# Optimization experiments

Hardware: AMD Instinct MI355X
Metric: run time of the kernel (lower is better)

## Reference

```python
import jax, jax.numpy as jnp
import numpy as np

N = 100_000          # nodes
E = 3_200_000        # train edges (avg degree 32)
E_TEST = 500_000     # pos/neg test edges each
F_IN, F_HID, F_OUT = 256, 16, 64


def setup_inputs() -> dict:
    key = jax.random.key(0)
    ks = jax.random.split(key, 7)
    x = jax.random.normal(ks[0], (N, F_IN), jnp.float32)
    train_edge_index = jax.random.randint(ks[1], (2, E), 0, N, dtype=jnp.int32)
    test_pos_edge_index = jax.random.randint(ks[2], (2, E_TEST), 0, N, dtype=jnp.int32)
    test_neg_edge_index = jax.random.randint(ks[3], (2, E_TEST), 0, N, dtype=jnp.int32)
    W1 = jax.random.normal(ks[4], (F_IN, F_HID), jnp.float32) / np.float32(np.sqrt(F_IN))
    b1 = jnp.zeros((F_HID,), jnp.float32)
    W2 = jax.random.normal(ks[5], (F_HID, F_OUT), jnp.float32) / np.float32(np.sqrt(F_HID))
    b2 = jnp.zeros((F_OUT,), jnp.float32)
    return dict(x=x, train_edge_index=train_edge_index,
                test_pos_edge_index=test_pos_edge_index,
                test_neg_edge_index=test_neg_edge_index,
                W1=W1, b1=b1, W2=W2, b2=b2)


def gcn_conv(x, edge_index, W, b, n):
    """PyG GCNConv: x' = D^-1/2 (A+I) D^-1/2 (x W) + b (self-loops added)."""
    h = x @ W                                  # project first (PyG order)
    loop = jnp.arange(n, dtype=edge_index.dtype)
    src = jnp.concatenate([edge_index[0], loop])
    dst = jnp.concatenate([edge_index[1], loop])
    deg = jax.ops.segment_sum(jnp.ones_like(dst, dtype=h.dtype), dst, num_segments=n)
    dinv = jnp.where(deg > 0, jax.lax.rsqrt(deg), 0.0)
    norm = dinv[src] * dinv[dst]               # per-edge symmetric norm
    msg = h[src] * norm[:, None]               # gather + scale
    out = jax.ops.segment_sum(msg, dst, num_segments=n)  # scatter-add
    return out + b


def reference(x, train_edge_index, test_pos_edge_index, test_neg_edge_index,
              W1, b1, W2, b2):
    n = x.shape[0]
    z = gcn_conv(x, train_edge_index, W1, b1, n)
    z = jax.nn.relu(z)
    z = gcn_conv(z, train_edge_index, W2, b2, n)
    edge_index = jnp.concatenate([test_pos_edge_index, test_neg_edge_index], axis=-1)
    logits = jnp.sum(z[edge_index[0]] * z[edge_index[1]], axis=-1)
    return logits
```

## Files before the change

kernel.cpp:

```cpp
#include <hip/hip_runtime.h>


#define CAP   18432
#define CHUNK 4096

__global__ void seed_kernel(int* __restrict__ gtail, int nb1) {
    int t = blockIdx.x * blockDim.x + threadIdx.x;
    if (t < nb1) gtail[t] = t * CAP;
}

__global__ void prep_kernel(const float* __restrict__ W2, const float* __restrict__ b2,
                            float* __restrict__ mw) {
    int t = threadIdx.x;
    int r = t >> 4, cc = t & 15;
    float s = 0.0f;
    for (int j = 0; j < 64; ++j) s += W2[r * 64 + j] * W2[cc * 64 + j];
    mw[t] = s;
    if (t < 16) {
        float w = 0.0f;
        for (int j = 0; j < 64; ++j) w += W2[t * 64 + j] * b2[j];
        mw[256 + t] = w;
    }
    if (t == 0) {
        float bbv = 0.0f;
        for (int j = 0; j < 64; ++j) bbv += b2[j] * b2[j];
        mw[272] = bbv;
    }
}

__global__ void passA1_kernel(const int* __restrict__ src, const int* __restrict__ dst, int E,
                              int* __restrict__ gtail, unsigned* __restrict__ tmp, int nb1) {
    __shared__ int cnt[256];
    __shared__ int base[256];
    int t = threadIdx.x;
    int c0 = blockIdx.x * CHUNK;
    if (t < nb1) cnt[t] = 0;
    __syncthreads();
    unsigned rec[16];
    unsigned brk[16];
    #pragma unroll
    for (int j = 0; j < 16; ++j) {
        int e = c0 + t + j * 256;
        if (e < E) {
            int s = src[e], d = dst[e];
            int b = d >> 9;
            int r = atomicAdd(&cnt[b], 1);
            rec[j] = (unsigned)s | ((unsigned)(d & 511) << 20);
            brk[j] = ((unsigned)b << 16) | (unsigned)r;
        }
    }
    __syncthreads();
    if (t < nb1) base[t] = atomicAdd(&gtail[t], cnt[t]);
    __syncthreads();
    #pragma unroll
    for (int j = 0; j < 16; ++j) {
        int e = c0 + t + j * 256;
        if (e < E) {
            int b = (int)(brk[j] >> 16), r = (int)(brk[j] & 0xFFFFu);
            tmp[base[b] + r] = rec[j];
        }
    }
}

__global__ void fill2_kernel(const int* __restrict__ gtail, const unsigned* __restrict__ tmp,
                             int* __restrict__ eidx, int* __restrict__ rowptr,
                             int* __restrict__ counts, float* __restrict__ dinv, int n) {
    int b = blockIdx.x;
    int t = threadIdx.x;
    int beg = b * CAP;
    int cnt_total = gtail[b] - beg;
    __shared__ int h[512];
    __shared__ int cur[512];
    h[t] = 0; h[t + 256] = 0;
    __syncthreads();
    for (int i = t; i < cnt_total; i += 256) {
        unsigned r = tmp[beg + i];
        atomicAdd(&h[r >> 20], 1);
    }
    __syncthreads();
    if (t == 0) {
        int run = beg;
        for (int j = 0; j < 512; ++j) { int c = h[j]; cur[j] = run; run += c; }
    }
    __syncthreads();
    for (int j = t; j < 512; j += 256) {
        int v = (b << 9) + j;
        if (v < n) {
            rowptr[v] = cur[j];
            counts[v] = h[j];
            dinv[v]   = rsqrtf((float)h[j] + 1.0f);
        }
    }
    __syncthreads();
    for (int i = t; i < cnt_total; i += 256) {
        unsigned r = tmp[beg + i];
        int p = atomicAdd(&cur[r >> 20], 1);
        eidx[p] = (int)(r & 0xFFFFF);
    }
}

__global__ void gemm1_kernel(const float* __restrict__ x, const float* __restrict__ W1,
                             const float* __restrict__ dinv, float* __restrict__ hs, int n) {
    __shared__ float4 sW[1024];
    const float4* W14 = (const float4*)W1;
    for (int i = threadIdx.x; i < 1024; i += 256) sW[i] = W14[i];
    __syncthreads();
    int row = blockIdx.x * 256 + threadIdx.x;
    if (row >= n) return;
    const float4* x4 = (const float4*)(x + (size_t)row * 256);
    float4 a0 = {0,0,0,0}, a1 = {0,0,0,0}, a2 = {0,0,0,0}, a3 = {0,0,0,0};
    for (int k4 = 0; k4 < 64; ++k4) {
        float4 xv = x4[k4];
        #pragma unroll
        for (int j = 0; j < 4; ++j) {
            float xk = (j == 0) ? xv.x : (j == 1) ? xv.y : (j == 2) ? xv.z : xv.w;
            int k = (k4 << 2) + j;
            float4 w0 = sW[k * 4 + 0];
            float4 w1 = sW[k * 4 + 1];
            float4 w2 = sW[k * 4 + 2];
            float4 w3 = sW[k * 4 + 3];
            a0.x += xk * w0.x; a0.y += xk * w0.y; a0.z += xk * w0.z; a0.w += xk * w0.w;
            a1.x += xk * w1.x; a1.y += xk * w1.y; a1.z += xk * w1.z; a1.w += xk * w1.w;
            a2.x += xk * w2.x; a2.y += xk * w2.y; a2.z += xk * w2.z; a2.w += xk * w2.w;
            a3.x += xk * w3.x; a3.y += xk * w3.y; a3.z += xk * w3.z; a3.w += xk * w3.w;
        }
    }
    float di = dinv[row];
    float4* o = (float4*)(hs + (size_t)row * 16);
    a0.x *= di; a0.y *= di; a0.z *= di; a0.w *= di;
    a1.x *= di; a1.y *= di; a1.z *= di; a1.w *= di;
    a2.x *= di; a2.y *= di; a2.z *= di; a2.w *= di;
    a3.x *= di; a3.y *= di; a3.z *= di; a3.w *= di;
    o[0] = a0; o[1] = a1; o[2] = a2; o[3] = a3;
}

__global__ void agg1_kernel(const int* __restrict__ rowptr, const int* __restrict__ counts,
                            const int* __restrict__ eidx, const float4* __restrict__ hs4,
                            const float* __restrict__ dinv, const float* __restrict__ b1,
                            float4* __restrict__ gs4, int n) {
    int t = blockIdx.x * blockDim.x + threadIdx.x;
    int v = t >> 3;
    if (v >= n) return;
    int q = t & 3, hh = (t >> 2) & 1;
    int start = rowptr[v], cnt = counts[v];
    float4 s = {0, 0, 0, 0};
    int i = hh;
    for (; i + 6 < cnt; i += 8) {
        int s0 = eidx[start + i];
        int s1 = eidx[start + i + 2];
        int s2 = eidx[start + i + 4];
        int s3 = eidx[start + i + 6];
        float4 h0 = hs4[(size_t)s0 * 4 + q];
        float4 h1 = hs4[(size_t)s1 * 4 + q];
        float4 h2 = hs4[(size_t)s2 * 4 + q];
        float4 h3 = hs4[(size_t)s3 * 4 + q];
        s.x += h0.x + h1.x + h2.x + h3.x;
        s.y += h0.y + h1.y + h2.y + h3.y;
        s.z += h0.z + h1.z + h2.z + h3.z;
        s.w += h0.w + h1.w + h2.w + h3.w;
    }
    for (; i < cnt; i += 2) {
        float4 h0 = hs4[(size_t)eidx[start + i] * 4 + q];
        s.x += h0.x; s.y += h0.y; s.z += h0.z; s.w += h0.w;
    }
    s.x += __shfl_xor(s.x, 4);
    s.y += __shfl_xor(s.y, 4);
    s.z += __shfl_xor(s.z, 4);
    s.w += __shfl_xor(s.w, 4);
    if (hh == 0) {
        float di = dinv[v];
        float4 h = hs4[(size_t)v * 4 + q];
        float4 b = ((const float4*)b1)[q];
        float4 z;
        z.x = fmaxf(di * (s.x + h.x) + b.x, 0.0f) * di;
        z.y = fmaxf(di * (s.y + h.y) + b.y, 0.0f) * di;
        z.z = fmaxf(di * (s.z + h.z) + b.z, 0.0f) * di;
        z.w = fmaxf(di * (s.w + h.w) + b.w, 0.0f) * di;
        gs4[(size_t)v * 4 + q] = z;
    }
}

__global__ void agg2y_kernel(const int* __restrict__ rowptr, const int* __restrict__ counts,
                             const int* __restrict__ eidx, const float4* __restrict__ gs4,
                             const float* __restrict__ dinv, const float* __restrict__ mw,
                             float4* __restrict__ u4, float* __restrict__ y,
                             float* __restrict__ c, int n) {
    __shared__ float su[32 * 16];
    __shared__ float sM[256];
    __shared__ float sw[16];
    int t = threadIdx.x;
    sM[t] = mw[t];
    if (t < 16) sw[t] = mw[256 + t];

    int j = t >> 3, q = t & 3, hh = (t >> 2) & 1;
    int v = blockIdx.x * 32 + j;
    if (v < n) {
        int start = rowptr[v], cnt = counts[v];
        float4 s = {0, 0, 0, 0};
        int i = hh;
        for (; i + 6 < cnt; i += 8) {
            int s0 = eidx[start + i];
            int s1 = eidx[start + i + 2];
            int s2 = eidx[start + i + 4];
            int s3 = eidx[start + i + 6];
            float4 g0 = gs4[(size_t)s0 * 4 + q];
            float4 g1 = gs4[(size_t)s1 * 4 + q];
            float4 g2 = gs4[(size_t)s2 * 4 + q];
            float4 g3 = gs4[(size_t)s3 * 4 + q];
            s.x += g0.x + g1.x + g2.x + g3.x;
            s.y += g0.y + g1.y + g2.y + g3.y;
            s.z += g0.z + g1.z + g2.z + g3.z;
            s.w += g0.w + g1.w + g2.w + g3.w;
        }
        for (; i < cnt; i += 2) {
            float4 g0 = gs4[(size_t)eidx[start + i] * 4 + q];
            s.x += g0.x; s.y += g0.y; s.z += g0.z; s.w += g0.w;
        }
        s.x += __shfl_xor(s.x, 4);
        s.y += __shfl_xor(s.y, 4);
        s.z += __shfl_xor(s.z, 4);
        s.w += __shfl_xor(s.w, 4);
        if (hh == 0) {
            float di = dinv[v];
            float4 g = gs4[(size_t)v * 4 + q];
            float4 uu;
            uu.x = di * (s.x + g.x);
            uu.y = di * (s.y + g.y);
            uu.z = di * (s.z + g.z);
            uu.w = di * (s.w + g.w);
            float* up = &su[j * 16 + q * 4];
            up[0] = uu.x; up[1] = uu.y; up[2] = uu.z; up[3] = uu.w;
            u4[(size_t)v * 4 + q] = uu;
        }
    }
    __syncthreads();
    if (v < n) {
        int l8 = t & 7;
        const float* uu = &su[j * 16];
        int c0 = l8 * 2;
        float y0 = sw[c0], y1 = sw[c0 + 1];
        #pragma unroll
        for (int k = 0; k < 16; ++k) {
            float uk = uu[k];
            y0 += uk * sM[k * 16 + c0];
            y1 += uk * sM[k * 16 + c0 + 1];
        }
        float2* yp = (float2*)(y + (size_t)v * 16 + c0);
        *yp = make_float2(y0, y1);
        if (l8 == 0) {
            float cv = 0.0f;
            #pragma unroll
            for (int k = 0; k < 16; ++k) cv += uu[k] * sw[k];
            c[v] = cv;
        }
    }
}

__global__ void edge_dot_kernel(const int* __restrict__ pa, const int* __restrict__ pb,
                                const int* __restrict__ na, const int* __restrict__ nb_,
                                int ET, const float* __restrict__ u, const float* __restrict__ y,
                                const float* __restrict__ c, const float* __restrict__ mw,
                                float* __restrict__ out) {
    int t = blockIdx.x * blockDim.x + threadIdx.x;
    int p = t >> 4, l = t & 15;
    if (p >= ET) return;
    int a0 = pa[p], b0 = pb[p];
    int a1 = na[p], b1 = nb_[p];
    float ya0 = y[(size_t)a0 * 16 + l];
    float ub0 = u[(size_t)b0 * 16 + l];
    float ya1 = y[(size_t)a1 * 16 + l];
    float ub1 = u[(size_t)b1 * 16 + l];
    float p0 = ya0 * ub0;
    float p1 = ya1 * ub1;
    p0 += __shfl_xor(p0, 1);  p1 += __shfl_xor(p1, 1);
    p0 += __shfl_xor(p0, 2);  p1 += __shfl_xor(p1, 2);
    p0 += __shfl_xor(p0, 4);  p1 += __shfl_xor(p1, 4);
    p0 += __shfl_xor(p0, 8);  p1 += __shfl_xor(p1, 8);
    if (l == 0) {
        float bb = mw[272];
        out[p]      = p0 + c[a0] + bb;
        out[ET + p] = p1 + c[a1] + bb;
    }
}

extern "C" void kernel_launch(void* const* d_in, const int* in_sizes, int n_in,
                              void* d_out, int out_size, void* d_ws, size_t ws_size,
                              hipStream_t stream) {
    const float* x    = (const float*)d_in[0];
    const int*   tei  = (const int*)d_in[1];
    const int*   tpos = (const int*)d_in[2];
    const int*   tneg = (const int*)d_in[3];
    const float* W1   = (const float*)d_in[4];
    const float* b1   = (const float*)d_in[5];
    const float* W2   = (const float*)d_in[6];
    const float* b2   = (const float*)d_in[7];
    float* out = (float*)d_out;

    int n   = in_sizes[0] / 256;
    int E   = in_sizes[1] / 2;
    int ET  = in_sizes[2] / 2;
    int nb1 = (n + 511) >> 9;

    char* w = (char*)d_ws;
    int*   gtail  = (int*)w;        w += 256 * 4;
    float* mw     = (float*)w;      w += 512 * 4;
    int*   rowptr = (int*)w;        w += (size_t)n * 4;
    int*   counts = (int*)w;        w += (size_t)n * 4;
    float* dinv   = (float*)w;      w += (size_t)n * 4;
    float* hs     = (float*)w;      w += (size_t)16 * n * 4;
    float* gs     = (float*)w;      w += (size_t)16 * n * 4;
    float* u      = (float*)w;      w += (size_t)16 * n * 4;
    float* y      = (float*)w;      w += (size_t)16 * n * 4;
    float* c      = (float*)w;      w += (size_t)n * 4;
    int*   eidx   = (int*)w;        w += (size_t)nb1 * CAP * 4;
    unsigned* tmp = (unsigned*)w;   w += (size_t)nb1 * CAP * 4;

    const int* src = tei;
    const int* dst = tei + E;

    seed_kernel<<<1, 256, 0, stream>>>(gtail, nb1);
    prep_kernel<<<1, 256, 0, stream>>>(W2, b2, mw);
    passA1_kernel<<<(E + CHUNK - 1) / CHUNK, 256, 0, stream>>>(src, dst, E, gtail, tmp, nb1);
    fill2_kernel<<<nb1, 256, 0, stream>>>(gtail, tmp, eidx, rowptr, counts, dinv, n);

    gemm1_kernel<<<(n + 255) / 256, 256, 0, stream>>>(x, W1, dinv, hs, n);
    agg1_kernel<<<(8 * n + 255) / 256, 256, 0, stream>>>(rowptr, counts, eidx,
                                                         (const float4*)hs, dinv, b1,
                                                         (float4*)gs, n);
    agg2y_kernel<<<(n + 31) / 32, 256, 0, stream>>>(rowptr, counts, eidx,
                                                    (const float4*)gs, dinv, mw,
                                                    (float4*)u, y, c, n);
    edge_dot_kernel<<<(16 * ET + 255) / 256, 256, 0, stream>>>(tpos, tpos + ET, tneg, tneg + ET,
                                                               ET, u, y, c, mw, out);
}
```

Baseline: 390.0 us.

## Stage x tiles in shared memory for gemm1 and merge seed/prep kernels

The first-layer GEMM now loads a 32-row tile of x into padded shared memory with coalesced float4 loads. Eight threads then cooperate per row, each computing two output columns. This replaces one thread per row reading its own 1 KB row, an uncoalesced strided access pattern, and it raises the block count. The seed and prep kernels are also merged into one launch to save launch overhead. The cost is more shared memory per block (about 49 KB), which may limit occupancy.

```diff
diff --git a/kernel.cpp b/kernel.cpp
--- a/kernel.cpp
+++ b/kernel.cpp
@@ -4,14 +4,11 @@
 #define CAP   18432
 #define CHUNK 4096
 
-__global__ void seed_kernel(int* __restrict__ gtail, int nb1) {
-    int t = blockIdx.x * blockDim.x + threadIdx.x;
+__global__ void seedprep_kernel(int* __restrict__ gtail, int nb1,
+                                const float* __restrict__ W2, const float* __restrict__ b2,
+                                float* __restrict__ mw) {
+    int t = threadIdx.x;
     if (t < nb1) gtail[t] = t * CAP;
-}
-
-__global__ void prep_kernel(const float* __restrict__ W2, const float* __restrict__ b2,
-                            float* __restrict__ mw) {
-    int t = threadIdx.x;
     int r = t >> 4, cc = t & 15;
     float s = 0.0f;
     for (int j = 0; j < 64; ++j) s += W2[r * 64 + j] * W2[cc * 64 + j];
@@ -101,37 +98,42 @@
 
 __global__ void gemm1_kernel(const float* __restrict__ x, const float* __restrict__ W1,
                              const float* __restrict__ dinv, float* __restrict__ hs, int n) {
-    __shared__ float4 sW[1024];
+    __shared__ float sx[32 * 260];
+    __shared__ float sw[4096];
+    int t = threadIdx.x;
     const float4* W14 = (const float4*)W1;
-    for (int i = threadIdx.x; i < 1024; i += 256) sW[i] = W14[i];
-    __syncthreads();
-    int row = blockIdx.x * 256 + threadIdx.x;
+    float4* sw4 = (float4*)sw;
+    for (int i = t; i < 1024; i += 256) sw4[i] = W14[i];
+    int rb = blockIdx.x * 32;
+    const float4* xg = (const float4*)x;
+    float4* sx4 = (float4*)sx;
+    #pragma unroll
+    for (int i = 0; i < 8; ++i) {
+        int f = t + 256 * i;
+        int row = rb + (f >> 6);
+        if (row < n) sx4[(f >> 6) * 65 + (f & 63)] = xg[(size_t)rb * 64 + f];
+    }
+    __syncthreads();
+    int rl = t >> 3;
+    int row = rb + rl;
     if (row >= n) return;
-    const float4* x4 = (const float4*)(x + (size_t)row * 256);
-    float4 a0 = {0,0,0,0}, a1 = {0,0,0,0}, a2 = {0,0,0,0}, a3 = {0,0,0,0};
+    int l8 = t & 7;
+    const float4* xr = &sx4[rl * 65];
+    const float2* sw2 = (const float2*)sw;
+    float a0 = 0.0f, a1 = 0.0f;
+    #pragma unroll 4
     for (int k4 = 0; k4 < 64; ++k4) {
-        float4 xv = x4[k4];
-        #pragma unroll
-        for (int j = 0; j < 4; ++j) {
-            float xk = (j == 0) ? xv.x : (j == 1) ? xv.y : (j == 2) ? xv.z : xv.w;
-            int k = (k4 << 2) + j;
-            float4 w0 = sW[k * 4 + 0];
-            float4 w1 = sW[k * 4 + 1];
-            float4 w2 = sW[k * 4 + 2];
-            float4 w3 = sW[k * 4 + 3];
-            a0.x += xk * w0.x; a0.y += xk * w0.y; a0.z += xk * w0.z; a0.w += xk * w0.w;
-            a1.x += xk * w1.x; a1.y += xk * w1.y; a1.z += xk * w1.z; a1.w += xk * w1.w;
-            a2.x += xk * w2.x; a2.y += xk * w2.y; a2.z += xk * w2.z; a2.w += xk * w2.w;
-            a3.x += xk * w3.x; a3.y += xk * w3.y; a3.z += xk * w3.z; a3.w += xk * w3.w;
-        }
+        float4 xv = xr[k4];
+        int k = k4 * 4;
+        float2 w0 = sw2[(k + 0) * 8 + l8];
+        float2 w1 = sw2[(k + 1) * 8 + l8];
+        float2 w2 = sw2[(k + 2) * 8 + l8];
+        float2 w3 = sw2[(k + 3) * 8 + l8];
+        a0 += xv.x * w0.x + xv.y * w1.x + xv.z * w2.x + xv.w * w3.x;
+        a1 += xv.x * w0.y + xv.y * w1.y + xv.z * w2.y + xv.w * w3.y;
     }
     float di = dinv[row];
-    float4* o = (float4*)(hs + (size_t)row * 16);
-    a0.x *= di; a0.y *= di; a0.z *= di; a0.w *= di;
-    a1.x *= di; a1.y *= di; a1.z *= di; a1.w *= di;
-    a2.x *= di; a2.y *= di; a2.z *= di; a2.w *= di;
-    a3.x *= di; a3.y *= di; a3.z *= di; a3.w *= di;
-    o[0] = a0; o[1] = a1; o[2] = a2; o[3] = a3;
+    *(float2*)(hs + (size_t)row * 16 + 2 * l8) = make_float2(a0 * di, a1 * di);
 }
 
 __global__ void agg1_kernel(const int* __restrict__ rowptr, const int* __restrict__ counts,
@@ -318,12 +320,11 @@
     const int* src = tei;
     const int* dst = tei + E;
 
-    seed_kernel<<<1, 256, 0, stream>>>(gtail, nb1);
-    prep_kernel<<<1, 256, 0, stream>>>(W2, b2, mw);
+    seedprep_kernel<<<1, 256, 0, stream>>>(gtail, nb1, W2, b2, mw);
     passA1_kernel<<<(E + CHUNK - 1) / CHUNK, 256, 0, stream>>>(src, dst, E, gtail, tmp, nb1);
     fill2_kernel<<<nb1, 256, 0, stream>>>(gtail, tmp, eidx, rowptr, counts, dinv, n);
 
-    gemm1_kernel<<<(n + 255) / 256, 256, 0, stream>>>(x, W1, dinv, hs, n);
+    gemm1_kernel<<<(n + 31) / 32, 256, 0, stream>>>(x, W1, dinv, hs, n);
     agg1_kernel<<<(8 * n + 255) / 256, 256, 0, stream>>>(rowptr, counts, eidx,
                                                          (const float4*)hs, dinv, b1,
                                                          (float4*)gs, n);
```

New measurement: 394.5 us. No clear change (+1.1%).
